# Kernel tuning notes

Hardware: AMD Instinct MI355X
Metric: run time of the kernel (lower is better)

## Reference

```python
import math
import jax, jax.numpy as jnp
import numpy as np

L_MAX = 3
PADDED = (1, 1, 2, 3)            # padded_l_list
K_MAX_L = (128, 96, 64, 32)      # channel bounds per l
FEATS = (32, 32, 32, 32)         # k_max_l[l] - k_max_l[l+1]
N_ATOMS = 20000
N_EDGES = 80000
N_RADIAL = 32
HIDDEN = 128
EPS = 1e-6


def setup_inputs() -> dict:
    key = jax.random.key(0)
    ks = jax.random.split(key, 40)
    it = iter(range(40))
    nk = lambda: ks[next(it)]
    inp = {}
    inp['rb'] = jax.random.normal(nk(), (L_MAX + 1, N_EDGES, N_RADIAL), jnp.float32)
    for l in range(L_MAX + 1):
        inp[f'sh{l}'] = jax.random.normal(nk(), (N_EDGES, 2 * l + 1), jnp.float32)
    for l in range(L_MAX + 1):
        P = PADDED[l]
        inp[f'f{l}'] = jax.random.normal(nk(), (N_ATOMS, P + 1, P + 1, FEATS[l]), jnp.float32)
    for P in (1, 2, 3):
        n = (P + 1) ** 2
        inp[f'U{P}'] = jax.random.normal(nk(), (n, n), jnp.float32) / math.sqrt(n)
    inp['gammas'] = jnp.ones((L_MAX + 1, 32), jnp.float32)
    inp['Win'] = jax.random.normal(nk(), (L_MAX + 1, 32, 32), jnp.float32) / math.sqrt(32.0)
    inp['Wout'] = jax.random.normal(nk(), (L_MAX + 1, 32, 32), jnp.float32) / math.sqrt(32.0)
    inp['A'] = jax.random.normal(nk(), (L_MAX + 1, N_RADIAL, HIDDEN), jnp.float32) / math.sqrt(float(N_RADIAL))
    for l in range(L_MAX + 1):
        inp[f'B{l}'] = jax.random.normal(nk(), (HIDDEN, K_MAX_L[l]), jnp.float32) / math.sqrt(float(HIDDEN))
    inp['msg_scale'] = jnp.float32(0.5)
    inp['centers'] = jax.random.randint(nk(), (N_EDGES,), 0, N_ATOMS)
    inp['neighbors'] = jax.random.randint(nk(), (N_EDGES,), 0, N_ATOMS)
    return inp


def _forward(rb, shs, feats, Us, gammas, Win, Wout, A, Bs, msg_scale, centers, neighbors):
    n_atoms = feats[0].shape[0]
    # EquivariantRMSNorm (norm over uncoupled i,j indices per channel) + linear_in
    h = []
    for l in range(L_MAX + 1):
        f = feats[l]
        rms = jnp.sqrt(jnp.mean(f * f, axis=(1, 2), keepdims=True) + EPS)
        fn = (f / rms) * gammas[l]
        h.append(jnp.einsum('nijf,fg->nijg', fn, Win[l]))
    # per-l radial MLP: [E, n_radial] -> silu -> [E, k_max_l[l]]
    rbm = [jax.nn.silu(rb[l] @ A[l]) @ Bs[l] for l in range(L_MAX + 1)]
    # vector expansion [E, 2l+1, k_max_l[l]]
    vexp = [shs[l][:, :, None] * rbm[l][:, None, :] for l in range(L_MAX + 1)]
    # split channels into per-l groups, uncouple via CG matrix U
    unc = []
    for l in range(L_MAX + 1):
        lower = K_MAX_L[l + 1] if l < L_MAX else 0
        upper = K_MAX_L[l]
        group = [vexp[lp][:, :, lower:upper] for lp in range(l + 1)]
        P = PADDED[l]
        if len(group) < P + 1:
            group.append(jnp.zeros((N_EDGES, 2 * P + 1, upper - lower), group[0].dtype))
        stacked = jnp.concatenate(group, axis=1)  # [E, (P+1)^2, feat]
        u = jnp.einsum('pq,eqf->epf', Us[P], stacked)
        unc.append(u.reshape(N_EDGES, P + 1, P + 1, upper - lower))
    # gather -> per-l tensor product -> scatter-add -> linear_out -> residual
    out = []
    for l in range(L_MAX + 1):
        P = PADDED[l]
        msg = jnp.einsum('eijf,ejkf->eikf', unc[l], h[l][neighbors]) / math.sqrt(P + 1.0)
        pooled = jnp.zeros((n_atoms,) + msg.shape[1:], msg.dtype).at[centers].add(msg) * msg_scale
        out.append(feats[l] + jnp.einsum('nijf,fg->nijg', pooled, Wout[l]))
    return tuple(out)


def reference(rb, sh0, sh1, sh2, sh3, f0, f1, f2, f3, U1, U2, U3, gammas, Win, Wout, A, B0, B1, B2, B3, msg_scale, centers, neighbors):
    return _forward(rb, [sh0, sh1, sh2, sh3], [f0, f1, f2, f3], {1: U1, 2: U2, 3: U3}, gammas, Win, Wout, A, [B0, B1, B2, B3], msg_scale, centers, neighbors)
```

## Files before the change

### kernel.cpp

```cpp
#include <hip/hip_runtime.h>
#include <cstdint>

#define NA 20000
#define NE 80000

typedef __attribute__((ext_vector_type(8))) short short8;
typedef __attribute__((ext_vector_type(4))) float f32x4;
typedef unsigned short ushort_t;

constexpr int HOFFc[4]   = {0, 2560000, 5120000, 10880000};
constexpr int RBMOFFc[4] = {0, 128, 224, 288};

__device__ __forceinline__ ushort_t f2bf(float x) {
    union { float f; unsigned u; } v; v.f = x;
    unsigned r = v.u + 0x7fffu + ((v.u >> 16) & 1u);
    return (ushort_t)(r >> 16);
}
__device__ __forceinline__ float bf2f(ushort_t u) {
    union { unsigned u; float f; } v; v.u = ((unsigned)u) << 16;
    return v.f;
}
__device__ __forceinline__ unsigned pack2(float a, float b) {
    return ((unsigned)f2bf(b) << 16) | (unsigned)f2bf(a);
}

__global__ __launch_bounds__(256)
void k_hist_prep(const int* __restrict__ centers, int* __restrict__ counts,
                 const float* __restrict__ B0, const float* __restrict__ B1,
                 const float* __restrict__ B2, const float* __restrict__ B3,
                 const float* __restrict__ A, const float* __restrict__ Win,
                 ushort_t* __restrict__ BT, ushort_t* __restrict__ ATb,
                 ushort_t* __restrict__ WinTb)
{
    const int b = blockIdx.x;
    if (b < 313) {
        const int e = b * 256 + threadIdx.x;
        if (e < NE) atomicAdd(&counts[centers[e]], 1);
        return;
    }
    const int i = (b - 313) * 256 + threadIdx.x;
    if (i < 40960) {
        const int n = i >> 7, k = i & 127;
        const float* src; int nl, N;
        if (n < 128)      { src = B0; nl = n;       N = 128; }
        else if (n < 224) { src = B1; nl = n - 128; N = 96;  }
        else if (n < 288) { src = B2; nl = n - 224; N = 64;  }
        else              { src = B3; nl = n - 288; N = 32;  }
        BT[i] = f2bf(src[k * N + nl]);
    } else if (i < 57344) {
        const int j2 = i - 40960;
        const int l = j2 >> 12, rem = j2 & 4095, jrow = rem >> 5, k = rem & 31;
        ATb[j2] = f2bf(A[l * 4096 + k * 128 + jrow]);
    } else if (i < 61440) {
        const int j3 = i - 57344;
        const int l = j3 >> 10, rem = j3 & 1023, g = rem >> 5, k = rem & 31;
        WinTb[j3] = f2bf(Win[l * 1024 + k * 32 + g]);
    }
}

template<int S, int AB>
__device__ __forceinline__ void norm_body(
    const float* __restrict__ fsel, const float* __restrict__ gammas, int l,
    const ushort_t* __restrict__ WinTb, ushort_t* __restrict__ hb,
    ushort_t* __restrict__ s_wt, float* __restrict__ s_scale)
{
    const int t = threadIdx.x;
    const int na0 = blockIdx.x * AB;

    if (t < 128) {
        reinterpret_cast<uint4*>(s_wt)[t] =
            reinterpret_cast<const uint4*>(WinTb + l * 1024)[t];
    }
    for (int i = t; i < AB * 32; i += 256) {
        const int a = i >> 5, c = i & 31;
        int aa = na0 + a; if (aa > NA - 1) aa = NA - 1;
        const float* fp = fsel + ((size_t)aa * S) * 32 + c;
        float ss = 0.f;
        #pragma unroll
        for (int s = 0; s < S; ++s) { const float v = fp[s * 32]; ss += v * v; }
        s_scale[i] = gammas[l * 32 + c] * rsqrtf(ss / (float)S + 1e-6f);
    }
    __syncthreads();

    const int w = t >> 6, lane = t & 63, l15 = lane & 15, lg = lane >> 4;
    const int row = w * 16 + l15;
    const bool rvalid = row < AB * S;
    const int rowc = rvalid ? row : 0;
    const int a = rowc / S, s = rowc % S;
    const int atom = na0 + a;
    const bool store_ok = rvalid && (atom < NA);
    const int atomc = (atom < NA) ? atom : (NA - 1);

    const float* fp = fsel + ((size_t)atomc * S + s) * 32 + lg * 8;
    const float4 x0 = *reinterpret_cast<const float4*>(fp);
    const float4 x1 = *reinterpret_cast<const float4*>(fp + 4);
    const float4 c0 = *reinterpret_cast<const float4*>(&s_scale[a * 32 + lg * 8]);
    const float4 c1 = *reinterpret_cast<const float4*>(&s_scale[a * 32 + lg * 8 + 4]);

    union { short8 v; unsigned u[4]; } bf;
    bf.u[0] = pack2(x0.x * c0.x, x0.y * c0.y);
    bf.u[1] = pack2(x0.z * c0.z, x0.w * c0.w);
    bf.u[2] = pack2(x1.x * c1.x, x1.y * c1.y);
    bf.u[3] = pack2(x1.z * c1.z, x1.w * c1.w);

    const short8 a0 = *reinterpret_cast<const short8*>(&s_wt[l15 * 32 + lg * 8]);
    const short8 a1 = *reinterpret_cast<const short8*>(&s_wt[(16 + l15) * 32 + lg * 8]);
    f32x4 d0 = __builtin_amdgcn_mfma_f32_16x16x32_bf16(a0, bf.v, (f32x4){0.f,0.f,0.f,0.f}, 0, 0, 0);
    f32x4 d1 = __builtin_amdgcn_mfma_f32_16x16x32_bf16(a1, bf.v, (f32x4){0.f,0.f,0.f,0.f}, 0, 0, 0);

    if (store_ok) {
        ushort_t* hp = hb + ((size_t)atomc * S + s) * 32;
        uint2 o0; o0.x = pack2(d0[0], d0[1]); o0.y = pack2(d0[2], d0[3]);
        uint2 o1; o1.x = pack2(d1[0], d1[1]); o1.y = pack2(d1[2], d1[3]);
        *reinterpret_cast<uint2*>(&hp[0  + 4 * lg]) = o0;
        *reinterpret_cast<uint2*>(&hp[16 + 4 * lg]) = o1;
    }
}

__global__ __launch_bounds__(256, 8)
void k_norm_mfma(const float* __restrict__ f0, const float* __restrict__ f1,
                 const float* __restrict__ f2, const float* __restrict__ f3,
                 const float* __restrict__ gammas, const ushort_t* __restrict__ WinTb,
                 ushort_t* __restrict__ h)
{
    __shared__ ushort_t s_wt[1024];
    __shared__ float s_scale[512];
    const int l = blockIdx.y;
    if (l == 0) {
        if (blockIdx.x >= 1250) return;
        norm_body<4, 16>(f0, gammas, 0, WinTb, h + HOFFc[0], s_wt, s_scale);
    } else if (l == 1) {
        if (blockIdx.x >= 1250) return;
        norm_body<4, 16>(f1, gammas, 1, WinTb, h + HOFFc[1], s_wt, s_scale);
    } else if (l == 2) {
        if (blockIdx.x >= 2858) return;
        norm_body<9, 7>(f2, gammas, 2, WinTb, h + HOFFc[2], s_wt, s_scale);
    } else {
        norm_body<16, 4>(f3, gammas, 3, WinTb, h + HOFFc[3], s_wt, s_scale);
    }
}

__global__ __launch_bounds__(256, 3)
void k_edgeA(const float* __restrict__ rb,
             const float* __restrict__ sh0, const float* __restrict__ sh1,
             const float* __restrict__ sh2, const float* __restrict__ sh3,
             const ushort_t* __restrict__ BT, const ushort_t* __restrict__ ATb,
             ushort_t* __restrict__ rbm, float* __restrict__ shq)
{
    __shared__ ushort_t s_h[8192];
    __shared__ ushort_t s_r2[16384];
    ushort_t* s_rbbf = s_r2;
    ushort_t* s_at   = s_r2 + 2048;
    ushort_t* s_bt   = s_r2;

    const int t  = threadIdx.x;
    const int e0 = blockIdx.x * 64;
    const int l  = blockIdx.y;
    const int w  = t >> 6, lane = t & 63;
    const int l15 = lane & 15, lg = lane >> 4;

    if (l == 0) {
        for (int i = t; i < 1024; i += 256) {
            const int q = i & 15, ge = e0 + (i >> 4);
            float v;
            if (q == 0)      v = sh0[ge];
            else if (q < 4)  v = sh1[ge * 3 + (q - 1)];
            else if (q < 9)  v = sh2[ge * 5 + (q - 4)];
            else             v = sh3[ge * 7 + (q - 9)];
            shq[(size_t)e0 * 16 + i] = v;
        }
    }

    const int Kl[4] = {128, 96, 64, 32};
    const int erow = w * 16 + l15;

    for (int i = t; i < 1024; i += 256) {
        const float2 v = *reinterpret_cast<const float2*>(
            &rb[(size_t)l * NE * 32 + (size_t)e0 * 32 + 2 * i]);
        *reinterpret_cast<unsigned*>(&s_rbbf[2 * i]) = pack2(v.x, v.y);
    }
    {
        const uint4* src = reinterpret_cast<const uint4*>(ATb + (size_t)l * 4096);
        for (int i = t; i < 512; i += 256) reinterpret_cast<uint4*>(s_at)[i] = src[i];
    }
    __syncthreads();

    const short8 rbf = *reinterpret_cast<const short8*>(&s_rbbf[erow * 32 + lg * 8]);
    #pragma unroll
    for (int jt = 0; jt < 8; ++jt) {
        const short8 af = *reinterpret_cast<const short8*>(&s_at[(jt * 16 + l15) * 32 + lg * 8]);
        f32x4 d = __builtin_amdgcn_mfma_f32_16x16x32_bf16(af, rbf, (f32x4){0.f,0.f,0.f,0.f}, 0, 0, 0);
        float s0 = d[0] / (1.f + __expf(-d[0]));
        float s1 = d[1] / (1.f + __expf(-d[1]));
        float s2 = d[2] / (1.f + __expf(-d[2]));
        float s3 = d[3] / (1.f + __expf(-d[3]));
        const int chunk = jt * 2 + (lg >> 1);
        const int base = erow * 128 + ((chunk ^ (erow & 7)) << 3) + (lg & 1) * 4;
        uint2 ov; ov.x = pack2(s0, s1); ov.y = pack2(s2, s3);
        *reinterpret_cast<uint2*>(&s_h[base]) = ov;
    }
    __syncthreads();

    const int K = Kl[l];
    for (int cch = t; cch < (K << 4); cch += 256) {
        const int n = cch >> 4, loc = cch & 15;
        const uint4 v = *reinterpret_cast<const uint4*>(&BT[(size_t)(RBMOFFc[l] + n) * 128 + loc * 8]);
        *reinterpret_cast<uint4*>(&s_bt[n * 128 + ((loc ^ (n & 7)) << 3)]) = v;
    }
    __syncthreads();

    const short8 hf0 = *reinterpret_cast<const short8*>(&s_h[erow * 128 + (((0 + lg) ^ (erow & 7)) << 3)]);
    const short8 hf1 = *reinterpret_cast<const short8*>(&s_h[erow * 128 + (((4 + lg) ^ (erow & 7)) << 3)]);
    const short8 hf2 = *reinterpret_cast<const short8*>(&s_h[erow * 128 + (((8 + lg) ^ (erow & 7)) << 3)]);
    const short8 hf3 = *reinterpret_cast<const short8*>(&s_h[erow * 128 + (((12 + lg) ^ (erow & 7)) << 3)]);

    const int ntn = K >> 4;
    for (int nt = 0; nt < ntn; ++nt) {
        const int n = nt * 16 + l15;
        f32x4 acc = {0.f, 0.f, 0.f, 0.f};
        #pragma unroll
        for (int ks = 0; ks < 4; ++ks) {
            const short8 af = *reinterpret_cast<const short8*>(
                &s_bt[n * 128 + (((ks * 4 + lg) ^ (n & 7)) << 3)]);
            const short8 hfk = (ks == 0) ? hf0 : (ks == 1) ? hf1 : (ks == 2) ? hf2 : hf3;
            acc = __builtin_amdgcn_mfma_f32_16x16x32_bf16(af, hfk, acc, 0, 0, 0);
        }
        uint2 ov;
        ov.x = pack2(acc[0], acc[1]);
        ov.y = pack2(acc[2], acc[3]);
        *reinterpret_cast<uint2*>(&rbm[(size_t)(e0 + erow) * 320 + RBMOFFc[l] + nt * 16 + 4 * lg]) = ov;
    }
}

__global__ __launch_bounds__(1024)
void k_scan(const int* __restrict__ counts, int* __restrict__ offsets)
{
    __shared__ int s_sum[1024];
    const int t = threadIdx.x;
    const int CH = 20;
    const int base = t * CH;
    int n = NA - base; n = n < 0 ? 0 : (n > CH ? CH : n);

    int tot = 0;
    for (int i = 0; i < n; i++) tot += counts[base + i];
    s_sum[t] = tot;
    __syncthreads();
    for (int off = 1; off < 1024; off <<= 1) {
        int v = (t >= off) ? s_sum[t - off] : 0;
        __syncthreads();
        s_sum[t] += v;
        __syncthreads();
    }
    int run = s_sum[t] - tot;
    for (int i = 0; i < n; i++) { offsets[base + i] = run; run += counts[base + i]; }
    if (t == 0) offsets[NA] = NE;
}

__global__ __launch_bounds__(256)
void k_fill(const int* __restrict__ centers, const int* __restrict__ offsets,
            int* __restrict__ cursor, int* __restrict__ elist)
{
    const int e = blockIdx.x * 256 + threadIdx.x;
    if (e < NE) {
        const int ctr = centers[e];
        const int pos = offsets[ctr] + atomicAdd(&cursor[ctr], 1);
        elist[pos] = e;
    }
}

template<int P1, int ASTART, int ACNT>
__device__ __forceinline__ void tp_step(float* __restrict__ acc,
                                        const float* __restrict__ lg,
                                        const ushort_t* __restrict__ lh,
                                        const float* __restrict__ rv, int c)
{
    float un[ACNT];
    #pragma unroll
    for (int pi = 0; pi < ACNT; ++pi) {
        const int p = ASTART + pi;
        float a = 0.f;
        #pragma unroll
        for (int lp = 0; lp < P1; ++lp) a += lg[p * 4 + lp] * rv[lp];
        un[pi] = a;
    }
    #pragma unroll
    for (int ii = 0; ii < ACNT / P1; ++ii) {
        #pragma unroll
        for (int k = 0; k < P1; ++k) {
            float m = 0.f;
            #pragma unroll
            for (int j = 0; j < P1; ++j) m += un[ii * P1 + j] * bf2f(lh[(j * P1 + k) * 32 + c]);
            acc[ii * P1 + k] += m;
        }
    }
}

template<int P1, int LOWER>
__device__ __forceinline__ void pool_big_body(
    const float* __restrict__ Up, float uscale,
    const float* __restrict__ WoutL, const float* __restrict__ msp,
    const float* __restrict__ shq, const ushort_t* __restrict__ rbm,
    const ushort_t* __restrict__ hL, const float* __restrict__ fL,
    float* __restrict__ outL,
    const int* __restrict__ offsets, const int* __restrict__ elist,
    const int* __restrict__ neighbors, float* __restrict__ sm)
{
    constexpr int S       = P1 * P1;
    constexpr int ACNT0   = (P1 == 4) ? 8 : 6;
    constexpr int ACNT1   = (P1 == 4) ? 8 : 3;
    constexpr int ASTART1 = ACNT0;
    constexpr int NV      = (S * 32) / 8;

    float*    s_U    = sm;
    float*    s_w    = sm + 256;
    ushort_t* s_hbuf = reinterpret_cast<ushort_t*>(sm + 256 + 1024);
    float*    s_gbuf = sm + 256 + 1024 + 128 * S;

    const int t = threadIdx.x;
    for (int i = t; i < S * S; i += 256) s_U[i] = Up[i] * uscale;
    for (int i = t; i < 1024; i += 256) s_w[i] = WoutL[i];
    __syncthreads();

    const int w = t >> 6, lane = t & 63, c = lane & 31, half = lane >> 5;
    const int n = blockIdx.x * 4 + w;
    const float ms = *msp;
    const int beg = offsets[n], end = offsets[n + 1];

    const int gp = lane >> 2, glp = lane & 3;
    const int qlo = (glp == 0) ? 0 : (glp == 1) ? 1 : (glp == 2) ? 4 : 9;
    const int qhi = (glp == 0) ? 1 : (glp == 1) ? 4 : (glp == 2) ? 9 : 16;
    const bool gvalid = (gp < S) && (glp < P1);

    float acc[ACNT0];
    #pragma unroll
    for (int x = 0; x < ACNT0; ++x) acc[x] = 0.f;

    ushort_t* lhA = s_hbuf + w * 2 * (S * 32);
    ushort_t* lhB = lhA + S * 32;
    float*    lgA = s_gbuf + w * 128;
    float*    lgB = lgA + 64;

    for (int slot = beg; slot < end; slot += 2) {
        const bool haveB = (slot + 1) < end;
        const int eA = elist[slot];
        const int eB = elist[haveB ? slot + 1 : slot];
        const int nbrA = neighbors[eA];
        const int nbrB = neighbors[eB];

        uint4 vA = {}, vB = {};
        const uint4* hpA = reinterpret_cast<const uint4*>(hL + (size_t)nbrA * (S * 32));
        const uint4* hpB = reinterpret_cast<const uint4*>(hL + (size_t)nbrB * (S * 32));
        if (lane < NV) { vA = hpA[lane]; vB = hpB[lane]; }

        const ushort_t* rrA = rbm + (size_t)eA * 320 + LOWER + c;
        const ushort_t* rrB = rbm + (size_t)eB * 320 + LOWER + c;
        float rvA[4], rvB[4];
        #pragma unroll
        for (int lp = 0; lp < P1; ++lp) { rvA[lp] = bf2f(rrA[RBMOFFc[lp]]); rvB[lp] = bf2f(rrB[RBMOFFc[lp]]); }

        const float* sqA = shq + (size_t)eA * 16;
        const float* sqB = shq + (size_t)eB * 16;
        float gA = 0.f, gB = 0.f;
        if (gvalid) {
            for (int q = qlo; q < qhi; ++q) {
                const float u = s_U[gp * S + q];
                gA += u * sqA[q];
                gB += u * sqB[q];
            }
        }

        if (lane < NV) {
            reinterpret_cast<uint4*>(lhA)[lane] = vA;
            reinterpret_cast<uint4*>(lhB)[lane] = vB;
        }
        lgA[lane] = gA;
        lgB[lane] = gB;

        asm volatile("s_waitcnt lgkmcnt(0)" ::: "memory");

        if (half == 0) tp_step<P1, 0,       ACNT0>(acc, lgA, lhA, rvA, c);
        else           tp_step<P1, ASTART1, ACNT1>(acc, lgA, lhA, rvA, c);
        if (haveB) {
            if (half == 0) tp_step<P1, 0,       ACNT0>(acc, lgB, lhB, rvB, c);
            else           tp_step<P1, ASTART1, ACNT1>(acc, lgB, lhB, rvB, c);
        }
    }

    float* accStage = reinterpret_cast<float*>(lhA);
    if (half == 0) {
        #pragma unroll
        for (int x = 0; x < ACNT0; ++x) accStage[x * 32 + c] = acc[x];
    } else {
        #pragma unroll
        for (int x = 0; x < ACNT1; ++x) accStage[(ASTART1 + x) * 32 + c] = acc[x];
    }
    asm volatile("s_waitcnt lgkmcnt(0)" ::: "memory");

    const float* fp = fL + (size_t)n * (S * 32);
    float* op = outL + (size_t)n * (S * 32);
    for (int s = half; s < S; s += 2) {
        float o = 0.f;
        #pragma unroll
        for (int f = 0; f < 32; f++) o += accStage[s * 32 + f] * s_w[f * 32 + c];
        op[s * 32 + c] = fp[s * 32 + c] + ms * o;
    }
}

__device__ __forceinline__ void pool_01_body(
    const float* __restrict__ U1, const float* __restrict__ Wout,
    const float* __restrict__ msp, const float* __restrict__ shq,
    const ushort_t* __restrict__ rbm, const ushort_t* __restrict__ h,
    const float* __restrict__ f0, const float* __restrict__ f1,
    float* __restrict__ out,
    const int* __restrict__ offsets, const int* __restrict__ elist,
    const int* __restrict__ neighbors, float* __restrict__ sm)
{
    float* s_U   = sm;
    float* s_w   = sm + 16;
    float* s_acc = sm + 16 + 2048;

    const int t = threadIdx.x;
    if (t < 16) s_U[t] = U1[t] * 0.70710678118654752f;
    for (int i = t; i < 2048; i += 256) s_w[i] = Wout[i];
    __syncthreads();

    const int w = t >> 6, lane = t & 63, c = lane & 31, half = lane >> 5;
    const int n = blockIdx.x * 4 + w;
    const float ms = *msp;
    const int beg = offsets[n], end = offsets[n + 1];
    const ushort_t* h0 = h;
    const ushort_t* h1 = h + 2560000;

    float acc0[4] = {0.f, 0.f, 0.f, 0.f};
    float acc1[4] = {0.f, 0.f, 0.f, 0.f};

    const int nit = (end - beg + 1) >> 1;
    for (int it = 0; it < nit; ++it) {
        const int slot = beg + it * 2 + half;
        const bool valid = slot < end;
        const int e   = elist[valid ? slot : beg];
        const int nbr = neighbors[e];
        const float fac = valid ? 1.f : 0.f;

        const ushort_t* rrow = rbm + (size_t)e * 320;
        const float rv0  = fac * bf2f(rrow[96 + c]);
        const float rv1a = fac * bf2f(rrow[64 + c]);
        const float rv1b = fac * bf2f(rrow[192 + c]);
        const float* sqp = shq + (size_t)e * 16;
        const float sq0 = sqp[0], sq1 = sqp[1], sq2 = sqp[2], sq3 = sqp[3];

        float hn0[4], hn1[4];
        const ushort_t* hp0 = h0 + (size_t)nbr * 128 + c;
        const ushort_t* hp1 = h1 + (size_t)nbr * 128 + c;
        #pragma unroll
        for (int p = 0; p < 4; ++p) { hn0[p] = bf2f(hp0[p * 32]); hn1[p] = bf2f(hp1[p * 32]); }

        const float st0 = sq0 * rv0;
        float st1[4];
        st1[0] = sq0 * rv1a; st1[1] = sq1 * rv1b; st1[2] = sq2 * rv1b; st1[3] = sq3 * rv1b;

        float unc0[4], unc1[4];
        #pragma unroll
        for (int p = 0; p < 4; ++p) {
            unc0[p] = s_U[p * 4] * st0;
            float a = 0.f;
            #pragma unroll
            for (int q = 0; q < 4; ++q) a += s_U[p * 4 + q] * st1[q];
            unc1[p] = a;
        }
        #pragma unroll
        for (int i = 0; i < 2; ++i) {
            #pragma unroll
            for (int k = 0; k < 2; ++k) {
                float m0 = 0.f, m1 = 0.f;
                #pragma unroll
                for (int j = 0; j < 2; ++j) {
                    m0 += unc0[i * 2 + j] * hn0[j * 2 + k];
                    m1 += unc1[i * 2 + j] * hn1[j * 2 + k];
                }
                acc0[i * 2 + k] += m0;
                acc1[i * 2 + k] += m1;
            }
        }
    }

    #pragma unroll
    for (int s = 0; s < 4; s++) { acc0[s] += __shfl_xor(acc0[s], 32); acc1[s] += __shfl_xor(acc1[s], 32); }
    #pragma unroll
    for (int s = 0; s < 4; s++) if ((s & 1) == half) {
        s_acc[(w * 2 + 0) * 128 + s * 32 + c] = acc0[s];
        s_acc[(w * 2 + 1) * 128 + s * 32 + c] = acc1[s];
    }
    __syncthreads();

    const float* fp0 = f0 + (size_t)n * 128;
    const float* fp1 = f1 + (size_t)n * 128;
    float* op0 = out + (size_t)n * 128;
    float* op1 = out + 2560000 + (size_t)n * 128;
    for (int s = half; s < 4; s += 2) {
        float o0 = 0.f, o1 = 0.f;
        #pragma unroll
        for (int f = 0; f < 32; f++) {
            o0 += s_acc[(w * 2 + 0) * 128 + s * 32 + f] * s_w[f * 32 + c];
            o1 += s_acc[(w * 2 + 1) * 128 + s * 32 + f] * s_w[1024 + f * 32 + c];
        }
        op0[s * 32 + c] = fp0[s * 32 + c] + ms * o0;
        op1[s * 32 + c] = fp1[s * 32 + c] + ms * o1;
    }
}

__global__ __launch_bounds__(256, 6)
void k_pools(const float* __restrict__ U1, const float* __restrict__ U2,
             const float* __restrict__ U3, const float* __restrict__ Wout,
             const float* __restrict__ msp, const float* __restrict__ shq,
             const ushort_t* __restrict__ rbm, const ushort_t* __restrict__ h,
             const float* __restrict__ f0, const float* __restrict__ f1,
             const float* __restrict__ f2, const float* __restrict__ f3,
             float* __restrict__ out,
             const int* __restrict__ offsets, const int* __restrict__ elist,
             const int* __restrict__ neighbors)
{
    __shared__ float sm[3840];
    const int which = blockIdx.y;
    if (which == 0) {
        pool_big_body<4, 0>(U3, 0.5f, Wout + 3072, msp, shq, rbm,
                            h + HOFFc[3], f3, out + HOFFc[3],
                            offsets, elist, neighbors, sm);
    } else if (which == 1) {
        pool_big_body<3, 32>(U2, 0.57735026918962576f, Wout + 2048, msp, shq, rbm,
                             h + HOFFc[2], f2, out + HOFFc[2],
                             offsets, elist, neighbors, sm);
    } else {
        pool_01_body(U1, Wout, msp, shq, rbm, h, f0, f1, out,
                     offsets, elist, neighbors, sm);
    }
}

extern "C" void kernel_launch(void* const* d_in, const int* in_sizes, int n_in,
                              void* d_out, int out_size, void* d_ws, size_t ws_size,
                              hipStream_t stream)
{
    (void)in_sizes; (void)n_in; (void)out_size;

    const float* rb     = (const float*)d_in[0];
    const float* sh0    = (const float*)d_in[1];
    const float* sh1    = (const float*)d_in[2];
    const float* sh2    = (const float*)d_in[3];
    const float* sh3    = (const float*)d_in[4];
    const float* f0     = (const float*)d_in[5];
    const float* f1     = (const float*)d_in[6];
    const float* f2     = (const float*)d_in[7];
    const float* f3     = (const float*)d_in[8];
    const float* U1     = (const float*)d_in[9];
    const float* U2     = (const float*)d_in[10];
    const float* U3     = (const float*)d_in[11];
    const float* gammas = (const float*)d_in[12];
    const float* Win    = (const float*)d_in[13];
    const float* Wout   = (const float*)d_in[14];
    const float* A      = (const float*)d_in[15];
    const float* B0     = (const float*)d_in[16];
    const float* B1     = (const float*)d_in[17];
    const float* B2     = (const float*)d_in[18];
    const float* B3     = (const float*)d_in[19];
    const float* msp    = (const float*)d_in[20];
    const int* centers   = (const int*)d_in[21];
    const int* neighbors = (const int*)d_in[22];

    const size_t OFF_RBM = 42240000;
    const size_t OFF_SHQ = 93440000;
    const size_t OFF_BT  = 98560000;
    const size_t OFF_AT  = 98641920;
    const size_t OFF_WT  = 98674688;
    const size_t OFF_INT = 98682880;
    const size_t needed  = OFF_INT + (size_t)140001 * 4;
    if (ws_size < needed) return;

    ushort_t* h_bf  = (ushort_t*)d_ws;
    ushort_t* rbm   = (ushort_t*)((char*)d_ws + OFF_RBM);
    float*    shq   = (float*)((char*)d_ws + OFF_SHQ);
    ushort_t* BT    = (ushort_t*)((char*)d_ws + OFF_BT);
    ushort_t* ATb   = (ushort_t*)((char*)d_ws + OFF_AT);
    ushort_t* WinTb = (ushort_t*)((char*)d_ws + OFF_WT);
    int* ibase   = (int*)((char*)d_ws + OFF_INT);
    int* offsets = ibase;
    int* counts  = ibase + 20001;
    int* cursor  = ibase + 40001;
    int* elist   = ibase + 60001;

    hipMemsetAsync(counts, 0, (size_t)40000 * sizeof(int), stream);

    k_hist_prep<<<553, 256, 0, stream>>>(centers, counts, B0, B1, B2, B3, A, Win,
                                         BT, ATb, WinTb);
    k_scan<<<1, 1024, 0, stream>>>(counts, offsets);
    k_fill<<<313, 256, 0, stream>>>(centers, offsets, cursor, elist);

    dim3 gN(5000, 4);
    k_norm_mfma<<<gN, 256, 0, stream>>>(f0, f1, f2, f3, gammas, WinTb, h_bf);
    dim3 gE(1250, 4);
    k_edgeA<<<gE, 256, 0, stream>>>(rb, sh0, sh1, sh2, sh3, BT, ATb, rbm, shq);

    dim3 gP(5000, 3);
    k_pools<<<gP, 256, 0, stream>>>(U1, U2, U3, Wout, msp, shq, rbm, h_bf,
                                    f0, f1, f2, f3, (float*)d_out,
                                    offsets, elist, neighbors);
}
```

Measured before the change: 280.6 us.

## Split each atom's edge loop across two waves in big pooling kernels

Each block in the l=2/l=3 pooling path now handles two atoms instead of four. Two waves share one atom, interleaving its edge pairs, and their partial accumulators are reduced through shared memory before the output projection. The grid doubles, and the extra blocks in the l=0/1 path exit early. The aim is to shorten per-wave serial edge loops and improve latency hiding, at the cost of block-wide syncs and a shared-memory reduction.

```diff
diff --git a/kernel.cpp b/kernel.cpp
--- a/kernel.cpp
+++ b/kernel.cpp
@@ -322,7 +322,8 @@
     __syncthreads();
 
     const int w = t >> 6, lane = t & 63, c = lane & 31, half = lane >> 5;
-    const int n = blockIdx.x * 4 + w;
+    const int aw = w >> 1, wp = w & 1;
+    const int n = blockIdx.x * 2 + aw;
     const float ms = *msp;
     const int beg = offsets[n], end = offsets[n + 1];
 
@@ -340,7 +341,7 @@
     float*    lgA = s_gbuf + w * 128;
     float*    lgB = lgA + 64;
 
-    for (int slot = beg; slot < end; slot += 2) {
+    for (int slot = beg + 2 * wp; slot < end; slot += 4) {
         const bool haveB = (slot + 1) < end;
         const int eA = elist[slot];
         const int eB = elist[haveB ? slot + 1 : slot];
@@ -386,22 +387,35 @@
         }
     }
 
-    float* accStage = reinterpret_cast<float*>(lhA);
-    if (half == 0) {
-        #pragma unroll
-        for (int x = 0; x < ACNT0; ++x) accStage[x * 32 + c] = acc[x];
-    } else {
-        #pragma unroll
-        for (int x = 0; x < ACNT1; ++x) accStage[(ASTART1 + x) * 32 + c] = acc[x];
-    }
-    asm volatile("s_waitcnt lgkmcnt(0)" ::: "memory");
+    __syncthreads();
+    float* accf = reinterpret_cast<float*>(s_hbuf) + aw * (S * 32);
+    if (wp == 0) {
+        if (half == 0) {
+            #pragma unroll
+            for (int x = 0; x < ACNT0; ++x) accf[x * 32 + c] = acc[x];
+        } else {
+            #pragma unroll
+            for (int x = 0; x < ACNT1; ++x) accf[(ASTART1 + x) * 32 + c] = acc[x];
+        }
+    }
+    __syncthreads();
+    if (wp == 1) {
+        if (half == 0) {
+            #pragma unroll
+            for (int x = 0; x < ACNT0; ++x) accf[x * 32 + c] += acc[x];
+        } else {
+            #pragma unroll
+            for (int x = 0; x < ACNT1; ++x) accf[(ASTART1 + x) * 32 + c] += acc[x];
+        }
+    }
+    __syncthreads();
 
     const float* fp = fL + (size_t)n * (S * 32);
     float* op = outL + (size_t)n * (S * 32);
-    for (int s = half; s < S; s += 2) {
+    for (int s = wp * 2 + half; s < S; s += 4) {
         float o = 0.f;
         #pragma unroll
-        for (int f = 0; f < 32; f++) o += accStage[s * 32 + f] * s_w[f * 32 + c];
+        for (int f = 0; f < 32; f++) o += accf[s * 32 + f] * s_w[f * 32 + c];
         op[s * 32 + c] = fp[s * 32 + c] + ms * o;
     }
 }
@@ -531,6 +545,7 @@
                              h + HOFFc[2], f2, out + HOFFc[2],
                              offsets, elist, neighbors, sm);
     } else {
+        if (blockIdx.x >= 5000) return;
         pool_01_body(U1, Wout, msp, shq, rbm, h, f0, f1, out,
                      offsets, elist, neighbors, sm);
     }
@@ -599,7 +614,7 @@
     dim3 gE(1250, 4);
     k_edgeA<<<gE, 256, 0, stream>>>(rb, sh0, sh1, sh2, sh3, BT, ATb, rbm, shq);
 
-    dim3 gP(5000, 3);
+    dim3 gP(10000, 3);
     k_pools<<<gP, 256, 0, stream>>>(U1, U2, U3, Wout, msp, shq, rbm, h_bf,
                                     f0, f1, f2, f3, (float*)d_out,
                                     offsets, elist, neighbors);
```

After: 301.1 us. 1.07x slower.
